# Kernel optimization log

Measured on AMD Instinct MI355X. Metric: run time of the kernel, lower is better.

The kernel has to match this reference:

```python
import jax, jax.numpy as jnp
import numpy as np

N_NODES = 100000
N_EDGES = 1600000
H = 64
N_LAYERS = 3
NUM_APPS = max(1, N_LAYERS - 1)  # forward applies layer once, then while l>1 loop


def setup_inputs() -> dict:
    key = jax.random.key(0)
    k1, k2, k3, k4, k5 = jax.random.split(key, 5)
    features = jax.random.normal(k1, (N_NODES, H), dtype=jnp.float32)
    W = jax.random.normal(k2, (H, H), dtype=jnp.float32) / np.sqrt(H)
    b = jax.random.normal(k3, (H,), dtype=jnp.float32) * 0.01
    src = jax.random.randint(k4, (N_EDGES,), 0, N_NODES, dtype=jnp.int64)
    dst = jax.random.randint(k5, (N_EDGES,), 0, N_NODES, dtype=jnp.int64)
    return {"features": features, "W": W, "b": b, "src": src, "dst": dst}


def reference(features, W, b, src, dst):
    n = features.shape[0]
    ones = jnp.ones(src.shape[0], dtype=features.dtype)
    # DGL GraphConv norm='both': symmetric normalization, degrees clamped >= 1
    deg_out = jax.ops.segment_sum(ones, src, num_segments=n)
    deg_in = jax.ops.segment_sum(ones, dst, num_segments=n)
    inv_sqrt_out = jnp.clip(deg_out, 1.0, None) ** -0.5  # [N]
    inv_sqrt_in = jnp.clip(deg_in, 1.0, None) ** -0.5    # [N]

    h = features
    for _ in range(NUM_APPS):  # shared-weight GraphConv + ReLU, applied n_layers-1 times
        msg = (h * inv_sqrt_out[:, None])[src]                   # [E, H] gather
        agg = jax.ops.segment_sum(msg, dst, num_segments=n)      # [N, H] scatter-add
        h = jax.nn.relu((agg * inv_sqrt_in[:, None]) @ W + b)    # [N, H]
    return h
```

## Files before the change

### kernel.cpp

```cpp
#include <hip/hip_runtime.h>
#include <hip/hip_fp16.h>

#define N_NODES 100000
#define N_EDGES 1600000
#define HDIM 64
#define NPB 512
#define NPB_SHIFT 9
#define NBUCK 196
#define CAP 16384
#define NCHUNK 512
#define CHUNK (N_EDGES / NCHUNK)
#define DROWS 64
#define DENSE_BLOCKS ((N_NODES + DROWS - 1) / DROWS)

typedef float f4v __attribute__((ext_vector_type(4)));

__global__ void init_kernel(int* __restrict__ gcurD, int* __restrict__ gcurS) {
    int t = threadIdx.x;
    if (t < NBUCK) {
        gcurD[t] = t * CAP;
        gcurS[t] = t * CAP;
    }
}

__device__ inline uint2 f4_to_h4(float x, float y, float z, float w) {
    __half2 lo = __floats2half2_rn(x, y);
    __half2 hi = __floats2half2_rn(z, w);
    uint2 r;
    r.x = *(unsigned*)&lo;
    r.y = *(unsigned*)&hi;
    return r;
}

__global__ void place_kernel(const int* __restrict__ src, const int* __restrict__ dst,
                             int* __restrict__ gcurD, int* __restrict__ gcurS,
                             unsigned int* __restrict__ bufD, unsigned short* __restrict__ bufS) {
    __shared__ int hD[NBUCK], hS[NBUCK], curD[NBUCK], curS[NBUCK];
    int t = threadIdx.x, blk = blockIdx.x;
    for (int i = t; i < NBUCK; i += 256) { hD[i] = 0; hS[i] = 0; }
    __syncthreads();
    int e0 = blk * CHUNK;
    for (int i = t; i < CHUNK; i += 256) {
        atomicAdd(&hD[dst[e0 + i] >> NPB_SHIFT], 1);
        atomicAdd(&hS[src[e0 + i] >> NPB_SHIFT], 1);
    }
    __syncthreads();
    for (int i = t; i < NBUCK; i += 256) {
        curD[i] = hD[i] ? atomicAdd(&gcurD[i], hD[i]) : 0;
        curS[i] = hS[i] ? atomicAdd(&gcurS[i], hS[i]) : 0;
    }
    __syncthreads();
    for (int i = t; i < CHUNK; i += 256) {
        int s = src[e0 + i], d = dst[e0 + i];
        int pd = atomicAdd(&curD[d >> NPB_SHIFT], 1);
        bufD[pd] = (unsigned)s | ((unsigned)(d & (NPB - 1)) << 17);
        int ps = atomicAdd(&curS[s >> NPB_SHIFT], 1);
        bufS[ps] = (unsigned short)(s & (NPB - 1));
    }
}

__device__ __forceinline__ void dense_body512(int t, int r0,
                                              const float* __restrict__ h,
                                              const float* __restrict__ W,
                                              uint2* __restrict__ hw, int n) {
    __shared__ float Wlds[HDIM * HDIM];
    for (int i = t; i < HDIM * HDIM / 4; i += 512)
        ((f4v*)Wlds)[i] = ((const f4v*)W)[i];

    int r = t >> 3, gl = t & 7;
    int row = r0 + r;
    f4v a0 = {0.f, 0.f, 0.f, 0.f}, a1 = a0;
    if (row < n) {
        a0 = __builtin_nontemporal_load((const f4v*)h + (long long)row * 16 + gl * 2 + 0);
        a1 = __builtin_nontemporal_load((const f4v*)h + (long long)row * 16 + gl * 2 + 1);
    }
    __syncthreads();

    float acc0 = 0.f, acc1 = 0.f, acc2 = 0.f, acc3 = 0.f;
    float acc4 = 0.f, acc5 = 0.f, acc6 = 0.f, acc7 = 0.f;
    int gbase = (t & 63) & 56;

#pragma unroll
    for (int k = 0; k < HDIM; ++k) {
        float av = ((k >> 2) & 1) ? a1[k & 3] : a0[k & 3];
        float ak = __shfl(av, gbase + (k >> 3), 64);
        f4v w0 = ((const f4v*)Wlds)[k * 16 + gl * 2 + 0];
        f4v w1 = ((const f4v*)Wlds)[k * 16 + gl * 2 + 1];
        acc0 = fmaf(ak, w0.x, acc0); acc1 = fmaf(ak, w0.y, acc1);
        acc2 = fmaf(ak, w0.z, acc2); acc3 = fmaf(ak, w0.w, acc3);
        acc4 = fmaf(ak, w1.x, acc4); acc5 = fmaf(ak, w1.y, acc5);
        acc6 = fmaf(ak, w1.z, acc6); acc7 = fmaf(ak, w1.w, acc7);
    }

    if (row < n) {
        hw[(long long)row * 16 + gl * 2 + 0] = f4_to_h4(acc0, acc1, acc2, acc3);
        hw[(long long)row * 16 + gl * 2 + 1] = f4_to_h4(acc4, acc5, acc6, acc7);
    }
}

__global__ void bucket_dense_kernel(const unsigned int* __restrict__ bufD,
                                    const unsigned short* __restrict__ bufS,
                                    const int* __restrict__ gcurD, const int* __restrict__ gcurS,
                                    int* __restrict__ csr_src, int2* __restrict__ offs,
                                    float* __restrict__ inv_in, float* __restrict__ inv_out,
                                    const float* __restrict__ h, const float* __restrict__ W,
                                    uint2* __restrict__ hw, int n) {
    __shared__ int cnt[NPB], pre[NPB], cur[NPB];
    int t = threadIdx.x;
    int blk = blockIdx.x;
    if (blk < NBUCK) {
        int b = blk;
        int ebase = b * CAP;
        int ecnt  = gcurD[b] - ebase;
        cnt[t] = 0;
        __syncthreads();
        for (int i = t; i < ecnt; i += NPB)
            atomicAdd(&cnt[(int)(bufD[ebase + i] >> 17)], 1);
        __syncthreads();
        int v = cnt[t];
        pre[t] = v;
        __syncthreads();
        for (int off = 1; off < NPB; off <<= 1) {
            int x = (t >= off) ? pre[t - off] : 0;
            __syncthreads(); pre[t] += x; __syncthreads();
        }
        int excl = pre[t] - v;
        cur[t] = excl;
        int node = b * NPB + t;
        if (node < N_NODES) {
            offs[node] = make_int2(ebase + excl, ebase + excl + v);
            inv_in[node] = rsqrtf((float)max(v, 1));
        }
        __syncthreads();
        for (int i = t; i < ecnt; i += NPB) {
            unsigned en = bufD[ebase + i];
            int pos = atomicAdd(&cur[(int)(en >> 17)], 1);
            csr_src[ebase + pos] = (int)(en & 0x1FFFFu);
        }
    } else if (blk < 2 * NBUCK) {
        int b = blk - NBUCK;
        int ebase = b * CAP;
        int ecnt  = gcurS[b] - ebase;
        cnt[t] = 0;
        __syncthreads();
        for (int i = t; i < ecnt; i += NPB)
            atomicAdd(&cnt[(int)bufS[ebase + i]], 1);
        __syncthreads();
        int node = b * NPB + t;
        if (node < N_NODES) inv_out[node] = rsqrtf((float)max(cnt[t], 1));
    } else {
        dense_body512(t, (blk - 2 * NBUCK) * DROWS, h, W, hw, n);
    }
}

__global__ void gather_dense_kernel(const uint4* __restrict__ hw_in, const float* __restrict__ inv_in,
                                    const float* __restrict__ inv_out,
                                    const int2* __restrict__ offs, const int* __restrict__ csr_src,
                                    const float* __restrict__ bias, const float* __restrict__ W,
                                    uint2* __restrict__ hw_out, int n) {
    __shared__ float Wlds[HDIM * HDIM];
    int t = threadIdx.x;
    for (int i = t; i < HDIM * HDIM / 4; i += 256)
        ((f4v*)Wlds)[i] = ((const f4v*)W)[i];

    int wave = t >> 6, lane = t & 63;
    int g = lane >> 3, gl = lane & 7;
    int row = blockIdx.x * 32 + wave * 8 + g;

    float acc0 = 0.f, acc1 = 0.f, acc2 = 0.f, acc3 = 0.f;
    float acc4 = 0.f, acc5 = 0.f, acc6 = 0.f, acc7 = 0.f;

    int2 oe = offs[row];
    int start = oe.x, end = oe.y;
    int gbase = g << 3;

    int jb = start;
    int mm = end - jb; if (mm > 8) mm = 8;
    int sidx = (mm > 0 && gl < mm) ? csr_src[jb + gl] : 0;
    float sw = inv_out[sidx];

    while (jb < end) {
        int jb2 = jb + 8;
        int mm2 = end - jb2; if (mm2 > 8) mm2 = 8;
        int sidx2 = (jb2 < end && gl < mm2) ? csr_src[jb2 + gl] : 0;
        float sw2 = inv_out[sidx2];

        if (mm == 8) {
#pragma unroll
            for (int j = 0; j < 8; ++j) {
                int s = __shfl(sidx, gbase + j, 64);
                float w = __shfl(sw, gbase + j, 64);
                uint4 u = hw_in[(long long)s * 8 + gl];
                float2 f0 = __half22float2(*(__half2*)&u.x);
                float2 f1 = __half22float2(*(__half2*)&u.y);
                float2 f2 = __half22float2(*(__half2*)&u.z);
                float2 f3 = __half22float2(*(__half2*)&u.w);
                acc0 = fmaf(f0.x, w, acc0); acc1 = fmaf(f0.y, w, acc1);
                acc2 = fmaf(f1.x, w, acc2); acc3 = fmaf(f1.y, w, acc3);
                acc4 = fmaf(f2.x, w, acc4); acc5 = fmaf(f2.y, w, acc5);
                acc6 = fmaf(f3.x, w, acc6); acc7 = fmaf(f3.y, w, acc7);
            }
        } else {
            for (int j = 0; j < mm; ++j) {
                int s = __shfl(sidx, gbase + j, 64);
                float w = __shfl(sw, gbase + j, 64);
                uint4 u = hw_in[(long long)s * 8 + gl];
                float2 f0 = __half22float2(*(__half2*)&u.x);
                float2 f1 = __half22float2(*(__half2*)&u.y);
                float2 f2 = __half22float2(*(__half2*)&u.z);
                float2 f3 = __half22float2(*(__half2*)&u.w);
                acc0 = fmaf(f0.x, w, acc0); acc1 = fmaf(f0.y, w, acc1);
                acc2 = fmaf(f1.x, w, acc2); acc3 = fmaf(f1.y, w, acc3);
                acc4 = fmaf(f2.x, w, acc4); acc5 = fmaf(f2.y, w, acc5);
                acc6 = fmaf(f3.x, w, acc6); acc7 = fmaf(f3.y, w, acc7);
            }
        }
        jb = jb2; mm = mm2; sidx = sidx2; sw = sw2;
    }

    float sc = inv_in[row];
    float4 b0 = ((const float4*)bias)[gl * 2 + 0];
    float4 b1 = ((const float4*)bias)[gl * 2 + 1];
    f4v h0, h1;
    h0.x = fmaxf(fmaf(acc0, sc, b0.x), 0.f);
    h0.y = fmaxf(fmaf(acc1, sc, b0.y), 0.f);
    h0.z = fmaxf(fmaf(acc2, sc, b0.z), 0.f);
    h0.w = fmaxf(fmaf(acc3, sc, b0.w), 0.f);
    h1.x = fmaxf(fmaf(acc4, sc, b1.x), 0.f);
    h1.y = fmaxf(fmaf(acc5, sc, b1.y), 0.f);
    h1.z = fmaxf(fmaf(acc6, sc, b1.z), 0.f);
    h1.w = fmaxf(fmaf(acc7, sc, b1.w), 0.f);

    __syncthreads();

    float d0 = 0.f, d1 = 0.f, d2 = 0.f, d3 = 0.f;
    float d4 = 0.f, d5 = 0.f, d6 = 0.f, d7 = 0.f;
#pragma unroll
    for (int k = 0; k < HDIM; ++k) {
        float av = ((k >> 2) & 1) ? h1[k & 3] : h0[k & 3];
        float ak = __shfl(av, gbase + (k >> 3), 64);
        f4v w0 = ((const f4v*)Wlds)[k * 16 + gl * 2 + 0];
        f4v w1 = ((const f4v*)Wlds)[k * 16 + gl * 2 + 1];
        d0 = fmaf(ak, w0.x, d0); d1 = fmaf(ak, w0.y, d1);
        d2 = fmaf(ak, w0.z, d2); d3 = fmaf(ak, w0.w, d3);
        d4 = fmaf(ak, w1.x, d4); d5 = fmaf(ak, w1.y, d5);
        d6 = fmaf(ak, w1.z, d6); d7 = fmaf(ak, w1.w, d7);
    }

    hw_out[(long long)row * 16 + gl * 2 + 0] = f4_to_h4(d0, d1, d2, d3);
    hw_out[(long long)row * 16 + gl * 2 + 1] = f4_to_h4(d4, d5, d6, d7);
}

__global__ void gather_kernel(const uint4* __restrict__ hw, const float* __restrict__ inv_in,
                              const float* __restrict__ inv_out,
                              const int2* __restrict__ offs, const int* __restrict__ csr_src,
                              const float* __restrict__ bias, float* __restrict__ out, int n) {
    int t = threadIdx.x;
    int wave = t >> 6, lane = t & 63;
    int g = lane >> 3, gl = lane & 7;
    int row = blockIdx.x * 32 + wave * 8 + g;
    if (row >= n) return;

    float acc0 = 0.f, acc1 = 0.f, acc2 = 0.f, acc3 = 0.f;
    float acc4 = 0.f, acc5 = 0.f, acc6 = 0.f, acc7 = 0.f;

    int2 oe = offs[row];
    int start = oe.x, end = oe.y;
    int gbase = g << 3;

    int jb = start;
    int mm = end - jb; if (mm > 8) mm = 8;
    int sidx = (mm > 0 && gl < mm) ? csr_src[jb + gl] : 0;
    float sw = inv_out[sidx];

    while (jb < end) {
        int jb2 = jb + 8;
        int mm2 = end - jb2; if (mm2 > 8) mm2 = 8;
        int sidx2 = (jb2 < end && gl < mm2) ? csr_src[jb2 + gl] : 0;
        float sw2 = inv_out[sidx2];

        if (mm == 8) {
#pragma unroll
            for (int j = 0; j < 8; ++j) {
                int s = __shfl(sidx, gbase + j, 64);
                float w = __shfl(sw, gbase + j, 64);
                uint4 u = hw[(long long)s * 8 + gl];
                float2 f0 = __half22float2(*(__half2*)&u.x);
                float2 f1 = __half22float2(*(__half2*)&u.y);
                float2 f2 = __half22float2(*(__half2*)&u.z);
                float2 f3 = __half22float2(*(__half2*)&u.w);
                acc0 = fmaf(f0.x, w, acc0); acc1 = fmaf(f0.y, w, acc1);
                acc2 = fmaf(f1.x, w, acc2); acc3 = fmaf(f1.y, w, acc3);
                acc4 = fmaf(f2.x, w, acc4); acc5 = fmaf(f2.y, w, acc5);
                acc6 = fmaf(f3.x, w, acc6); acc7 = fmaf(f3.y, w, acc7);
            }
        } else {
            for (int j = 0; j < mm; ++j) {
                int s = __shfl(sidx, gbase + j, 64);
                float w = __shfl(sw, gbase + j, 64);
                uint4 u = hw[(long long)s * 8 + gl];
                float2 f0 = __half22float2(*(__half2*)&u.x);
                float2 f1 = __half22float2(*(__half2*)&u.y);
                float2 f2 = __half22float2(*(__half2*)&u.z);
                float2 f3 = __half22float2(*(__half2*)&u.w);
                acc0 = fmaf(f0.x, w, acc0); acc1 = fmaf(f0.y, w, acc1);
                acc2 = fmaf(f1.x, w, acc2); acc3 = fmaf(f1.y, w, acc3);
                acc4 = fmaf(f2.x, w, acc4); acc5 = fmaf(f2.y, w, acc5);
                acc6 = fmaf(f3.x, w, acc6); acc7 = fmaf(f3.y, w, acc7);
            }
        }
        jb = jb2; mm = mm2; sidx = sidx2; sw = sw2;
    }

    float sc = inv_in[row];
    float4 b0 = ((const float4*)bias)[gl * 2 + 0];
    float4 b1 = ((const float4*)bias)[gl * 2 + 1];
    f4v r0, r1;
    r0.x = fmaxf(fmaf(acc0, sc, b0.x), 0.f);
    r0.y = fmaxf(fmaf(acc1, sc, b0.y), 0.f);
    r0.z = fmaxf(fmaf(acc2, sc, b0.z), 0.f);
    r0.w = fmaxf(fmaf(acc3, sc, b0.w), 0.f);
    r1.x = fmaxf(fmaf(acc4, sc, b1.x), 0.f);
    r1.y = fmaxf(fmaf(acc5, sc, b1.y), 0.f);
    r1.z = fmaxf(fmaf(acc6, sc, b1.z), 0.f);
    r1.w = fmaxf(fmaf(acc7, sc, b1.w), 0.f);
    __builtin_nontemporal_store(r0, (f4v*)out + (long long)row * 16 + gl * 2 + 0);
    __builtin_nontemporal_store(r1, (f4v*)out + (long long)row * 16 + gl * 2 + 1);
}

extern "C" void kernel_launch(void* const* d_in, const int* in_sizes, int n_in,
                              void* d_out, int out_size, void* d_ws, size_t ws_size,
                              hipStream_t stream) {
    const float* features = (const float*)d_in[0];
    const float* W        = (const float*)d_in[1];
    const float* b        = (const float*)d_in[2];
    const int*   src      = (const int*)d_in[3];
    const int*   dst      = (const int*)d_in[4];

    float* out = (float*)d_out;

    float* ws = (float*)d_ws;
    uint2* hw  = (uint2*)ws;
    uint2* hw2 = (uint2*)(ws + (size_t)N_NODES * 32);
    unsigned int*   bufD = (unsigned int*)(ws + (size_t)N_NODES * 64);
    unsigned short* bufS = (unsigned short*)(bufD + (size_t)NBUCK * CAP);
    int*   csr_src = (int*)(bufS + (size_t)NBUCK * CAP);
    int2*  offs    = (int2*)(csr_src + (size_t)NBUCK * CAP);
    float* inv_out = (float*)(offs + N_NODES);
    float* inv_in  = inv_out + N_NODES;
    int*   gcurD   = (int*)(inv_in + N_NODES);
    int*   gcurS   = gcurD + NBUCK;

    const int N = N_NODES;
    int gather_blocks = (N + 31) / 32;

    init_kernel<<<1, 256, 0, stream>>>(gcurD, gcurS);

    place_kernel<<<NCHUNK, 256, 0, stream>>>(src, dst, gcurD, gcurS, bufD, bufS);

    bucket_dense_kernel<<<2 * NBUCK + DENSE_BLOCKS, NPB, 0, stream>>>(
        bufD, bufS, gcurD, gcurS, csr_src, offs, inv_in, inv_out,
        features, W, hw, N);

    gather_dense_kernel<<<gather_blocks, 256, 0, stream>>>(
        (const uint4*)hw, inv_in, inv_out, offs, csr_src, b, W, hw2, N);

    gather_kernel<<<gather_blocks, 256, 0, stream>>>(
        (const uint4*)hw2, inv_in, inv_out, offs, csr_src, b, out, N);
}
```

Measured before the change: 261.3 us.

## Fold source-degree normalization into dense outputs and count out-degrees with global atomics

Out-degrees are now counted directly with global atomics in the place kernel, so the source bucket buffer and the second set of bucket blocks go away. The inv_sqrt_out scaling is applied to each source row before the dense transform, and in the epilogue of the first gather layer, so the gather loops become plain adds with no per-edge weight load and no shuffle. The prefix scan now uses wave shuffles, edge index loads are nontemporal, and chunk and block sizes change. The trade-off is 1.6M global atomics on degS, which can contend, in place of bucketed counting.

```diff
diff --git a/kernel.cpp b/kernel.cpp
--- a/kernel.cpp
+++ b/kernel.cpp
@@ -8,19 +8,18 @@
 #define NPB_SHIFT 9
 #define NBUCK 196
 #define CAP 16384
-#define NCHUNK 512
+#define NCHUNK 256
 #define CHUNK (N_EDGES / NCHUNK)
+#define GBLK 3125
 #define DROWS 64
-#define DENSE_BLOCKS ((N_NODES + DROWS - 1) / DROWS)
+#define DBLK ((N_NODES + DROWS - 1) / DROWS)
 
 typedef float f4v __attribute__((ext_vector_type(4)));
 
-__global__ void init_kernel(int* __restrict__ gcurD, int* __restrict__ gcurS) {
-    int t = threadIdx.x;
-    if (t < NBUCK) {
-        gcurD[t] = t * CAP;
-        gcurS[t] = t * CAP;
-    }
+__global__ void init_kernel(int* __restrict__ gcurD, int* __restrict__ degS) {
+    int idx = blockIdx.x * 512 + threadIdx.x;
+    if (idx < N_NODES) degS[idx] = 0;
+    if (blockIdx.x == 0 && threadIdx.x < NBUCK) gcurD[threadIdx.x] = threadIdx.x * CAP;
 }
 
 __device__ inline uint2 f4_to_h4(float x, float y, float z, float w) {
@@ -33,82 +32,40 @@
 }
 
 __global__ void place_kernel(const int* __restrict__ src, const int* __restrict__ dst,
-                             int* __restrict__ gcurD, int* __restrict__ gcurS,
-                             unsigned int* __restrict__ bufD, unsigned short* __restrict__ bufS) {
-    __shared__ int hD[NBUCK], hS[NBUCK], curD[NBUCK], curS[NBUCK];
+                             int* __restrict__ gcurD, int* __restrict__ degS,
+                             unsigned int* __restrict__ bufD) {
+    __shared__ int hD[NBUCK], curD[NBUCK];
     int t = threadIdx.x, blk = blockIdx.x;
-    for (int i = t; i < NBUCK; i += 256) { hD[i] = 0; hS[i] = 0; }
+    for (int i = t; i < NBUCK; i += 512) hD[i] = 0;
     __syncthreads();
     int e0 = blk * CHUNK;
-    for (int i = t; i < CHUNK; i += 256) {
+    for (int i = t; i < CHUNK; i += 512) {
         atomicAdd(&hD[dst[e0 + i] >> NPB_SHIFT], 1);
-        atomicAdd(&hS[src[e0 + i] >> NPB_SHIFT], 1);
+        atomicAdd(&degS[src[e0 + i]], 1);
     }
     __syncthreads();
-    for (int i = t; i < NBUCK; i += 256) {
+    for (int i = t; i < NBUCK; i += 512)
         curD[i] = hD[i] ? atomicAdd(&gcurD[i], hD[i]) : 0;
-        curS[i] = hS[i] ? atomicAdd(&gcurS[i], hS[i]) : 0;
-    }
     __syncthreads();
-    for (int i = t; i < CHUNK; i += 256) {
+    for (int i = t; i < CHUNK; i += 512) {
         int s = src[e0 + i], d = dst[e0 + i];
         int pd = atomicAdd(&curD[d >> NPB_SHIFT], 1);
         bufD[pd] = (unsigned)s | ((unsigned)(d & (NPB - 1)) << 17);
-        int ps = atomicAdd(&curS[s >> NPB_SHIFT], 1);
-        bufS[ps] = (unsigned short)(s & (NPB - 1));
-    }
-}
-
-__device__ __forceinline__ void dense_body512(int t, int r0,
-                                              const float* __restrict__ h,
-                                              const float* __restrict__ W,
-                                              uint2* __restrict__ hw, int n) {
-    __shared__ float Wlds[HDIM * HDIM];
-    for (int i = t; i < HDIM * HDIM / 4; i += 512)
-        ((f4v*)Wlds)[i] = ((const f4v*)W)[i];
-
-    int r = t >> 3, gl = t & 7;
-    int row = r0 + r;
-    f4v a0 = {0.f, 0.f, 0.f, 0.f}, a1 = a0;
-    if (row < n) {
-        a0 = __builtin_nontemporal_load((const f4v*)h + (long long)row * 16 + gl * 2 + 0);
-        a1 = __builtin_nontemporal_load((const f4v*)h + (long long)row * 16 + gl * 2 + 1);
-    }
-    __syncthreads();
-
-    float acc0 = 0.f, acc1 = 0.f, acc2 = 0.f, acc3 = 0.f;
-    float acc4 = 0.f, acc5 = 0.f, acc6 = 0.f, acc7 = 0.f;
-    int gbase = (t & 63) & 56;
-
-#pragma unroll
-    for (int k = 0; k < HDIM; ++k) {
-        float av = ((k >> 2) & 1) ? a1[k & 3] : a0[k & 3];
-        float ak = __shfl(av, gbase + (k >> 3), 64);
-        f4v w0 = ((const f4v*)Wlds)[k * 16 + gl * 2 + 0];
-        f4v w1 = ((const f4v*)Wlds)[k * 16 + gl * 2 + 1];
-        acc0 = fmaf(ak, w0.x, acc0); acc1 = fmaf(ak, w0.y, acc1);
-        acc2 = fmaf(ak, w0.z, acc2); acc3 = fmaf(ak, w0.w, acc3);
-        acc4 = fmaf(ak, w1.x, acc4); acc5 = fmaf(ak, w1.y, acc5);
-        acc6 = fmaf(ak, w1.z, acc6); acc7 = fmaf(ak, w1.w, acc7);
-    }
-
-    if (row < n) {
-        hw[(long long)row * 16 + gl * 2 + 0] = f4_to_h4(acc0, acc1, acc2, acc3);
-        hw[(long long)row * 16 + gl * 2 + 1] = f4_to_h4(acc4, acc5, acc6, acc7);
     }
 }
 
 __global__ void bucket_dense_kernel(const unsigned int* __restrict__ bufD,
-                                    const unsigned short* __restrict__ bufS,
-                                    const int* __restrict__ gcurD, const int* __restrict__ gcurS,
+                                    const int* __restrict__ gcurD,
                                     int* __restrict__ csr_src, int2* __restrict__ offs,
-                                    float* __restrict__ inv_in, float* __restrict__ inv_out,
+                                    float* __restrict__ inv_in,
+                                    const int* __restrict__ degS,
                                     const float* __restrict__ h, const float* __restrict__ W,
                                     uint2* __restrict__ hw, int n) {
-    __shared__ int cnt[NPB], pre[NPB], cur[NPB];
     int t = threadIdx.x;
     int blk = blockIdx.x;
     if (blk < NBUCK) {
+        __shared__ int cnt[NPB], cur[NPB];
+        __shared__ int wsum[8];
         int b = blk;
         int ebase = b * CAP;
         int ecnt  = gcurD[b] - ebase;
@@ -118,13 +75,19 @@
             atomicAdd(&cnt[(int)(bufD[ebase + i] >> 17)], 1);
         __syncthreads();
         int v = cnt[t];
-        pre[t] = v;
-        __syncthreads();
-        for (int off = 1; off < NPB; off <<= 1) {
-            int x = (t >= off) ? pre[t - off] : 0;
-            __syncthreads(); pre[t] += x; __syncthreads();
-        }
-        int excl = pre[t] - v;
+        int lane = t & 63, w = t >> 6;
+        int p = v;
+#pragma unroll
+        for (int d = 1; d < 64; d <<= 1) {
+            int x = __shfl_up(p, d, 64);
+            if (lane >= d) p += x;
+        }
+        if (lane == 63) wsum[w] = p;
+        __syncthreads();
+        int base = 0;
+#pragma unroll
+        for (int i = 0; i < 8; ++i) base += (i < w) ? wsum[i] : 0;
+        int excl = base + p - v;
         cur[t] = excl;
         int node = b * NPB + t;
         if (node < N_NODES) {
@@ -137,24 +100,58 @@
             int pos = atomicAdd(&cur[(int)(en >> 17)], 1);
             csr_src[ebase + pos] = (int)(en & 0x1FFFFu);
         }
-    } else if (blk < 2 * NBUCK) {
-        int b = blk - NBUCK;
-        int ebase = b * CAP;
-        int ecnt  = gcurS[b] - ebase;
-        cnt[t] = 0;
-        __syncthreads();
-        for (int i = t; i < ecnt; i += NPB)
-            atomicAdd(&cnt[(int)bufS[ebase + i]], 1);
-        __syncthreads();
-        int node = b * NPB + t;
-        if (node < N_NODES) inv_out[node] = rsqrtf((float)max(cnt[t], 1));
     } else {
-        dense_body512(t, (blk - 2 * NBUCK) * DROWS, h, W, hw, n);
-    }
-}
+        __shared__ float Wlds[HDIM * HDIM];
+        for (int i = t; i < HDIM * HDIM / 4; i += 512)
+            ((f4v*)Wlds)[i] = ((const f4v*)W)[i];
+
+        int r = t >> 3, gl = t & 7;
+        int row = (blk - NBUCK) * DROWS + r;
+        f4v a0 = {0.f, 0.f, 0.f, 0.f}, a1 = a0;
+        if (row < n) {
+            float so = rsqrtf((float)max(degS[row], 1));
+            a0 = __builtin_nontemporal_load((const f4v*)h + (long long)row * 16 + gl * 2 + 0);
+            a1 = __builtin_nontemporal_load((const f4v*)h + (long long)row * 16 + gl * 2 + 1);
+            a0.x *= so; a0.y *= so; a0.z *= so; a0.w *= so;
+            a1.x *= so; a1.y *= so; a1.z *= so; a1.w *= so;
+        }
+        __syncthreads();
+
+        float acc0 = 0.f, acc1 = 0.f, acc2 = 0.f, acc3 = 0.f;
+        float acc4 = 0.f, acc5 = 0.f, acc6 = 0.f, acc7 = 0.f;
+        int gbase = (t & 63) & 56;
+
+#pragma unroll
+        for (int k = 0; k < HDIM; ++k) {
+            float av = ((k >> 2) & 1) ? a1[k & 3] : a0[k & 3];
+            float ak = __shfl(av, gbase + (k >> 3), 64);
+            f4v w0 = ((const f4v*)Wlds)[k * 16 + gl * 2 + 0];
+            f4v w1 = ((const f4v*)Wlds)[k * 16 + gl * 2 + 1];
+            acc0 = fmaf(ak, w0.x, acc0); acc1 = fmaf(ak, w0.y, acc1);
+            acc2 = fmaf(ak, w0.z, acc2); acc3 = fmaf(ak, w0.w, acc3);
+            acc4 = fmaf(ak, w1.x, acc4); acc5 = fmaf(ak, w1.y, acc5);
+            acc6 = fmaf(ak, w1.z, acc6); acc7 = fmaf(ak, w1.w, acc7);
+        }
+
+        if (row < n) {
+            hw[(long long)row * 16 + gl * 2 + 0] = f4_to_h4(acc0, acc1, acc2, acc3);
+            hw[(long long)row * 16 + gl * 2 + 1] = f4_to_h4(acc4, acc5, acc6, acc7);
+        }
+    }
+}
+
+#define ACC8(u)                                              \
+    {                                                        \
+        float2 f0 = __half22float2(*(__half2*)&(u).x);       \
+        float2 f1 = __half22float2(*(__half2*)&(u).y);       \
+        float2 f2 = __half22float2(*(__half2*)&(u).z);       \
+        float2 f3 = __half22float2(*(__half2*)&(u).w);       \
+        acc0 += f0.x; acc1 += f0.y; acc2 += f1.x; acc3 += f1.y; \
+        acc4 += f2.x; acc5 += f2.y; acc6 += f3.x; acc7 += f3.y; \
+    }
 
 __global__ void gather_dense_kernel(const uint4* __restrict__ hw_in, const float* __restrict__ inv_in,
-                                    const float* __restrict__ inv_out,
+                                    const int* __restrict__ degS,
                                     const int2* __restrict__ offs, const int* __restrict__ csr_src,
                                     const float* __restrict__ bias, const float* __restrict__ W,
                                     uint2* __restrict__ hw_out, int n) {
@@ -176,60 +173,43 @@
 
     int jb = start;
     int mm = end - jb; if (mm > 8) mm = 8;
-    int sidx = (mm > 0 && gl < mm) ? csr_src[jb + gl] : 0;
-    float sw = inv_out[sidx];
+    int sidx = (mm > 0 && gl < mm) ? __builtin_nontemporal_load(csr_src + jb + gl) : 0;
 
     while (jb < end) {
         int jb2 = jb + 8;
         int mm2 = end - jb2; if (mm2 > 8) mm2 = 8;
-        int sidx2 = (jb2 < end && gl < mm2) ? csr_src[jb2 + gl] : 0;
-        float sw2 = inv_out[sidx2];
+        int sidx2 = (jb2 < end && gl < mm2) ? __builtin_nontemporal_load(csr_src + jb2 + gl) : 0;
 
         if (mm == 8) {
 #pragma unroll
             for (int j = 0; j < 8; ++j) {
                 int s = __shfl(sidx, gbase + j, 64);
-                float w = __shfl(sw, gbase + j, 64);
                 uint4 u = hw_in[(long long)s * 8 + gl];
-                float2 f0 = __half22float2(*(__half2*)&u.x);
-                float2 f1 = __half22float2(*(__half2*)&u.y);
-                float2 f2 = __half22float2(*(__half2*)&u.z);
-                float2 f3 = __half22float2(*(__half2*)&u.w);
-                acc0 = fmaf(f0.x, w, acc0); acc1 = fmaf(f0.y, w, acc1);
-                acc2 = fmaf(f1.x, w, acc2); acc3 = fmaf(f1.y, w, acc3);
-                acc4 = fmaf(f2.x, w, acc4); acc5 = fmaf(f2.y, w, acc5);
-                acc6 = fmaf(f3.x, w, acc6); acc7 = fmaf(f3.y, w, acc7);
+                ACC8(u)
             }
         } else {
             for (int j = 0; j < mm; ++j) {
                 int s = __shfl(sidx, gbase + j, 64);
-                float w = __shfl(sw, gbase + j, 64);
                 uint4 u = hw_in[(long long)s * 8 + gl];
-                float2 f0 = __half22float2(*(__half2*)&u.x);
-                float2 f1 = __half22float2(*(__half2*)&u.y);
-                float2 f2 = __half22float2(*(__half2*)&u.z);
-                float2 f3 = __half22float2(*(__half2*)&u.w);
-                acc0 = fmaf(f0.x, w, acc0); acc1 = fmaf(f0.y, w, acc1);
-                acc2 = fmaf(f1.x, w, acc2); acc3 = fmaf(f1.y, w, acc3);
-                acc4 = fmaf(f2.x, w, acc4); acc5 = fmaf(f2.y, w, acc5);
-                acc6 = fmaf(f3.x, w, acc6); acc7 = fmaf(f3.y, w, acc7);
+                ACC8(u)
             }
         }
-        jb = jb2; mm = mm2; sidx = sidx2; sw = sw2;
+        jb = jb2; mm = mm2; sidx = sidx2;
     }
 
     float sc = inv_in[row];
+    float so = rsqrtf((float)max(degS[row], 1));
     float4 b0 = ((const float4*)bias)[gl * 2 + 0];
     float4 b1 = ((const float4*)bias)[gl * 2 + 1];
     f4v h0, h1;
-    h0.x = fmaxf(fmaf(acc0, sc, b0.x), 0.f);
-    h0.y = fmaxf(fmaf(acc1, sc, b0.y), 0.f);
-    h0.z = fmaxf(fmaf(acc2, sc, b0.z), 0.f);
-    h0.w = fmaxf(fmaf(acc3, sc, b0.w), 0.f);
-    h1.x = fmaxf(fmaf(acc4, sc, b1.x), 0.f);
-    h1.y = fmaxf(fmaf(acc5, sc, b1.y), 0.f);
-    h1.z = fmaxf(fmaf(acc6, sc, b1.z), 0.f);
-    h1.w = fmaxf(fmaf(acc7, sc, b1.w), 0.f);
+    h0.x = fmaxf(fmaf(acc0, sc, b0.x), 0.f) * so;
+    h0.y = fmaxf(fmaf(acc1, sc, b0.y), 0.f) * so;
+    h0.z = fmaxf(fmaf(acc2, sc, b0.z), 0.f) * so;
+    h0.w = fmaxf(fmaf(acc3, sc, b0.w), 0.f) * so;
+    h1.x = fmaxf(fmaf(acc4, sc, b1.x), 0.f) * so;
+    h1.y = fmaxf(fmaf(acc5, sc, b1.y), 0.f) * so;
+    h1.z = fmaxf(fmaf(acc6, sc, b1.z), 0.f) * so;
+    h1.w = fmaxf(fmaf(acc7, sc, b1.w), 0.f) * so;
 
     __syncthreads();
 
@@ -252,7 +232,6 @@
 }
 
 __global__ void gather_kernel(const uint4* __restrict__ hw, const float* __restrict__ inv_in,
-                              const float* __restrict__ inv_out,
                               const int2* __restrict__ offs, const int* __restrict__ csr_src,
                               const float* __restrict__ bias, float* __restrict__ out, int n) {
     int t = threadIdx.x;
@@ -265,51 +244,32 @@
     float acc4 = 0.f, acc5 = 0.f, acc6 = 0.f, acc7 = 0.f;
 
     int2 oe = offs[row];
-    int start = oe.x, end = oe.y;
+    int jb = oe.x, end = oe.y;
     int gbase = g << 3;
 
-    int jb = start;
     int mm = end - jb; if (mm > 8) mm = 8;
-    int sidx = (mm > 0 && gl < mm) ? csr_src[jb + gl] : 0;
-    float sw = inv_out[sidx];
+    int sidx = (mm > 0 && gl < mm) ? __builtin_nontemporal_load(csr_src + jb + gl) : 0;
 
     while (jb < end) {
         int jb2 = jb + 8;
         int mm2 = end - jb2; if (mm2 > 8) mm2 = 8;
-        int sidx2 = (jb2 < end && gl < mm2) ? csr_src[jb2 + gl] : 0;
-        float sw2 = inv_out[sidx2];
+        int sidx2 = (jb2 < end && gl < mm2) ? __builtin_nontemporal_load(csr_src + jb2 + gl) : 0;
 
         if (mm == 8) {
 #pragma unroll
             for (int j = 0; j < 8; ++j) {
                 int s = __shfl(sidx, gbase + j, 64);
-                float w = __shfl(sw, gbase + j, 64);
                 uint4 u = hw[(long long)s * 8 + gl];
-                float2 f0 = __half22float2(*(__half2*)&u.x);
-                float2 f1 = __half22float2(*(__half2*)&u.y);
-                float2 f2 = __half22float2(*(__half2*)&u.z);
-                float2 f3 = __half22float2(*(__half2*)&u.w);
-                acc0 = fmaf(f0.x, w, acc0); acc1 = fmaf(f0.y, w, acc1);
-                acc2 = fmaf(f1.x, w, acc2); acc3 = fmaf(f1.y, w, acc3);
-                acc4 = fmaf(f2.x, w, acc4); acc5 = fmaf(f2.y, w, acc5);
-                acc6 = fmaf(f3.x, w, acc6); acc7 = fmaf(f3.y, w, acc7);
+                ACC8(u)
             }
         } else {
             for (int j = 0; j < mm; ++j) {
                 int s = __shfl(sidx, gbase + j, 64);
-                float w = __shfl(sw, gbase + j, 64);
                 uint4 u = hw[(long long)s * 8 + gl];
-                float2 f0 = __half22float2(*(__half2*)&u.x);
-                float2 f1 = __half22float2(*(__half2*)&u.y);
-                float2 f2 = __half22float2(*(__half2*)&u.z);
-                float2 f3 = __half22float2(*(__half2*)&u.w);
-                acc0 = fmaf(f0.x, w, acc0); acc1 = fmaf(f0.y, w, acc1);
-                acc2 = fmaf(f1.x, w, acc2); acc3 = fmaf(f1.y, w, acc3);
-                acc4 = fmaf(f2.x, w, acc4); acc5 = fmaf(f2.y, w, acc5);
-                acc6 = fmaf(f3.x, w, acc6); acc7 = fmaf(f3.y, w, acc7);
+                ACC8(u)
             }
         }
-        jb = jb2; mm = mm2; sidx = sidx2; sw = sw2;
+        jb = jb2; mm = mm2; sidx = sidx2;
     }
 
     float sc = inv_in[row];
@@ -342,29 +302,25 @@
     float* ws = (float*)d_ws;
     uint2* hw  = (uint2*)ws;
     uint2* hw2 = (uint2*)(ws + (size_t)N_NODES * 32);
-    unsigned int*   bufD = (unsigned int*)(ws + (size_t)N_NODES * 64);
-    unsigned short* bufS = (unsigned short*)(bufD + (size_t)NBUCK * CAP);
-    int*   csr_src = (int*)(bufS + (size_t)NBUCK * CAP);
+    unsigned int* bufD = (unsigned int*)(ws + (size_t)N_NODES * 64);
+    int*   csr_src = (int*)(bufD + (size_t)NBUCK * CAP);
     int2*  offs    = (int2*)(csr_src + (size_t)NBUCK * CAP);
-    float* inv_out = (float*)(offs + N_NODES);
-    float* inv_in  = inv_out + N_NODES;
-    int*   gcurD   = (int*)(inv_in + N_NODES);
-    int*   gcurS   = gcurD + NBUCK;
+    float* inv_in  = (float*)(offs + N_NODES);
+    int*   degS    = (int*)(inv_in + N_NODES);
+    int*   gcurD   = degS + N_NODES;
 
     const int N = N_NODES;
-    int gather_blocks = (N + 31) / 32;
-
-    init_kernel<<<1, 256, 0, stream>>>(gcurD, gcurS);
-
-    place_kernel<<<NCHUNK, 256, 0, stream>>>(src, dst, gcurD, gcurS, bufD, bufS);
-
-    bucket_dense_kernel<<<2 * NBUCK + DENSE_BLOCKS, NPB, 0, stream>>>(
-        bufD, bufS, gcurD, gcurS, csr_src, offs, inv_in, inv_out,
-        features, W, hw, N);
-
-    gather_dense_kernel<<<gather_blocks, 256, 0, stream>>>(
-        (const uint4*)hw, inv_in, inv_out, offs, csr_src, b, W, hw2, N);
-
-    gather_kernel<<<gather_blocks, 256, 0, stream>>>(
-        (const uint4*)hw2, inv_in, inv_out, offs, csr_src, b, out, N);
-}
+
+    init_kernel<<<196, 512, 0, stream>>>(gcurD, degS);
+
+    place_kernel<<<NCHUNK, 512, 0, stream>>>(src, dst, gcurD, degS, bufD);
+
+    bucket_dense_kernel<<<NBUCK + DBLK, 512, 0, stream>>>(
+        bufD, gcurD, csr_src, offs, inv_in, degS, features, W, hw, N);
+
+    gather_dense_kernel<<<GBLK, 256, 0, stream>>>(
+        (const uint4*)hw, inv_in, degS, offs, csr_src, b, W, hw2, N);
+
+    gather_kernel<<<GBLK, 256, 0, stream>>>(
+        (const uint4*)hw2, inv_in, offs, csr_src, b, out, N);
+}
```

Result: slower. 284.6 us (+8.9%).
